# Performance work log

Measured on AMD Instinct MI355X. Metric: run time of the kernel, lower is better.

## Reference

```python
import jax
jax.config.update("jax_enable_x64", True)  # codes use *1e12 factors; need int64
import jax.numpy as jnp
import numpy as np

# HashRectsPt hyperparameters (module buffers)
W0, H0 = 512.0, 512.0
ALPHA = 1.2
GAMMA = 0.6
BX, BY = 0.5, 0.5
N_RECTS = 8192


def setup_inputs() -> dict:
    key = jax.random.key(0)
    k1, k2, k3 = jax.random.split(key, 3)
    xy = jax.random.uniform(k1, (N_RECTS, 2), minval=0.0, maxval=2000.0)
    wh = jax.random.uniform(k2, (N_RECTS, 2), minval=8.0, maxval=512.0)
    rects = jnp.concatenate([xy, wh], axis=1).astype(jnp.float32)  # [N,4] x,y,w,h
    conf = jax.random.uniform(k3, (N_RECTS,), dtype=jnp.float32)
    return {"rects": rects, "conf": conf}


def _hash_codes(rects):
    # HashRectsPt.__call__ -> packed single int64 code per rect
    x, y, w, h = rects[:, 0], rects[:, 1], rects[:, 2], rects[:, 3]
    log_alpha = jnp.log(jnp.float32(ALPHA))
    i = jnp.round((jnp.log(jnp.float32(W0)) - jnp.log(w)) / log_alpha)
    j = jnp.round((jnp.log(jnp.float32(H0)) - jnp.log(h)) / log_alpha)
    gamma_ratio = (1.0 - GAMMA) / (1.0 + GAMMA)
    di = (W0 * gamma_ratio) / (ALPHA ** i)
    dj = (H0 * gamma_ratio) / (ALPHA ** j)
    # b_is_relative=True branch
    qx = jnp.round(x / di - BX)
    qy = jnp.round(y / dj - BY)
    codes = (qx.astype(jnp.int64)
             + qy.astype(jnp.int64) * 10_000
             + i.astype(jnp.int64) * 100_000_000
             + j.astype(jnp.int64) * 1_000_000_000_000)
    return codes  # [N] int64


def reference(rects, conf):
    codes = _hash_codes(rects)                         # [N]
    n = codes.shape[0]
    # torch.unique with data-dependent U -> padded fixed-size unique (U<=N);
    # pad value can never equal a real code, so padded columns match nothing.
    uniq = jnp.unique(codes, size=n, fill_value=jnp.iinfo(jnp.int64).min)  # [N]
    assign = codes[:, None] == uniq[None, :]           # [N, U] bool
    scores = conf[:, None] * assign.astype(conf.dtype)  # [N, U]
    # torch .max(dim=0) returns first max index; jnp.argmax matches.
    argidx = jnp.argmax(scores, axis=0)                # [U]
    return argidx
```

## Files before the change

### kernel.cpp

```cpp
#include <hip/hip_runtime.h>
#include <math.h>

#define N     8192
#define TBL   16384
#define TBLM  16383

__device__ __forceinline__ unsigned int hash_code32(float x, float y, float w, float h) {
    const float LOG_ALPHA = (float)log((double)1.2f);
    const float LOGW0     = (float)log(512.0);
    float i_f = rintf((LOGW0 - (float)log((double)w)) / LOG_ALPHA);
    float j_f = rintf((LOGW0 - (float)log((double)h)) / LOG_ALPHA);
    float pi  = (float)pow((double)1.2f, (double)i_f);
    float pj  = (float)pow((double)1.2f, (double)j_f);
    float qx  = rintf(x / (128.0f / pi) - 0.5f);
    float qy  = rintf(y / (128.0f / pj) - 0.5f);
    return (unsigned int)qx
         | ((unsigned int)qy  << 11)
         | ((unsigned int)i_f << 22)
         | ((unsigned int)j_f << 27);
}

__device__ __forceinline__ unsigned int hslot(unsigned int code) {
    return (code * 2654435761u) >> 18;
}

__global__ void __launch_bounds__(256)
k_init(const float4* __restrict__ rects, const float* __restrict__ conf,
       unsigned long long* __restrict__ v64,
       unsigned int* __restrict__ tcode, unsigned long long* __restrict__ tkey,
       unsigned int* __restrict__ compact, unsigned int* __restrict__ cnt,
       int* __restrict__ out) {
    int gt = blockIdx.x * 256 + threadIdx.x;
    tcode[gt] = 0u;
    tkey[gt]  = 0ULL;
    if (gt < N) {
        float4 r = rects[gt];
        unsigned int code = hash_code32(r.x, r.y, r.z, r.w);
        v64[gt] = ((unsigned long long)code << 32)
                | (unsigned long long)__float_as_uint(conf[gt]);
        out[gt]     = 0;
        compact[gt] = 0xFFFFFFFFu;
    }
    if (gt == 0) *cnt = 0u;
}

__global__ void __launch_bounds__(64)
k_insert(const unsigned long long* __restrict__ v64,
         unsigned int* __restrict__ tcode,
         unsigned long long* __restrict__ tkey,
         unsigned int* __restrict__ compact,
         unsigned int* __restrict__ cnt) {
    int i = blockIdx.x * 64 + threadIdx.x;
    int lane = threadIdx.x;
    unsigned long long v = v64[i];
    unsigned int code = (unsigned int)(v >> 32);
    unsigned int tag  = code + 1u;
    unsigned int h = hslot(code);
    bool claimed = false;
    for (;;) {
        unsigned int prev = atomicCAS(&tcode[h], 0u, tag);
        if (prev == 0u) { claimed = true; break; }
        if (prev == tag) break;
        h = (h + 1) & TBLM;
    }
    atomicMax(&tkey[h], (v << 32) | (unsigned int)(N - 1 - i));
    unsigned long long mask = __ballot(claimed);
    if (mask) {
        int leader = __ffsll((long long)mask) - 1;
        unsigned int base = 0;
        if (lane == leader)
            base = atomicAdd(cnt, (unsigned int)__popcll(mask));
        base = (unsigned int)__shfl((int)base, leader);
        if (claimed) {
            unsigned int off = (unsigned int)__popcll(
                mask & ((1ULL << lane) - 1ULL));
            compact[base + off] = code;
        }
    }
}

__global__ void __launch_bounds__(512)
k_rank(const unsigned long long* __restrict__ v64,
       const unsigned int* __restrict__ tcode,
       const unsigned long long* __restrict__ tkey,
       const unsigned int* __restrict__ compact,
       int* __restrict__ out) {
    __shared__ unsigned int s_ci[32];
    __shared__ int s_part[8][32];
    const int t = threadIdx.x;
    const int b = blockIdx.x;
    if (t < 32) s_ci[t] = (unsigned int)(v64[b * 32 + t] >> 32);
    __syncthreads();

    const int g    = t >> 7;
    const int lt   = t & 127;
    const int wave = t >> 6;

    unsigned int ci[8];
    #pragma unroll
    for (int q = 0; q < 8; ++q)
        ci[q] = __builtin_amdgcn_readfirstlane(s_ci[g * 8 + q]);

    int r[8] = {0, 0, 0, 0, 0, 0, 0, 0};
    const uint4* c4 = (const uint4*)compact;
    #pragma unroll
    for (int k = 0; k < 16; ++k) {
        uint4 e = c4[lt + k * 128];
        #pragma unroll
        for (int q = 0; q < 8; ++q) {
            r[q] += (int)(e.x < ci[q]) + (int)(e.y < ci[q])
                  + (int)(e.z < ci[q]) + (int)(e.w < ci[q]);
        }
    }
    #pragma unroll
    for (int q = 0; q < 8; ++q) {
        r[q] += __shfl_xor(r[q], 1);
        r[q] += __shfl_xor(r[q], 2);
        r[q] += __shfl_xor(r[q], 4);
        r[q] += __shfl_xor(r[q], 8);
        r[q] += __shfl_xor(r[q], 16);
        r[q] += __shfl_xor(r[q], 32);
    }
    if ((t & 63) == 0) {
        #pragma unroll
        for (int q = 0; q < 8; ++q)
            s_part[wave][(wave >> 1) * 8 + q] = r[q];
    }
    __syncthreads();

    if (t < 32) {
        int i = b * 32 + t;
        int gg = t >> 3;
        int rr = s_part[2 * gg][t] + s_part[2 * gg + 1][t];
        unsigned long long vi = v64[i];
        unsigned int cI = (unsigned int)(vi >> 32);
        unsigned int h = hslot(cI);
        while (tcode[h] != cI + 1u) h = (h + 1) & TBLM;
        if ((unsigned int)tkey[h] == (unsigned int)(N - 1 - i)) {
            out[rr] = ((unsigned int)vi == 0u) ? 0 : i;
        }
    }
}

extern "C" void kernel_launch(void* const* d_in, const int* in_sizes, int n_in,
                              void* d_out, int out_size, void* d_ws, size_t ws_size,
                              hipStream_t stream) {
    const float4* rects = (const float4*)d_in[0];
    const float*  conf  = (const float*)d_in[1];
    int* out = (int*)d_out;

    char* ws = (char*)d_ws;
    unsigned long long* v64     = (unsigned long long*)ws;
    unsigned int*       tcode   = (unsigned int*)(ws + 65536);
    unsigned long long* tkey    = (unsigned long long*)(ws + 131072);
    unsigned int*       compact = (unsigned int*)(ws + 262144);
    unsigned int*       cnt     = (unsigned int*)(ws + 294912);

    k_init  <<<TBL / 256, 256, 0, stream>>>(rects, conf, v64, tcode, tkey,
                                            compact, cnt, out);
    k_insert<<<N / 64, 64, 0, stream>>>(v64, tcode, tkey, compact, cnt);
    k_rank  <<<256, 512, 0, stream>>>(v64, tcode, tkey, compact, out);
}
```

Measured before the change: 73.16 us.

## Drop init kernel using epoch-tagged persistent hash tables and per-slot compact

Removes the separate initialization kernel by keeping the hash table and key table in persistent device globals tagged with an epoch counter derived from a launch counter, so stale entries from earlier calls are treated as empty instead of being cleared. Code computation and insertion are fused into one kernel. A shuffle-based lookup table of powers of 1.2 replaces per-thread double pow. The compaction atomic is replaced by writing each code at its own index, with the unique count derived in the rank kernel, which also zero-fills the tail of the output. This saves a launch and the table clears, at the cost of CAS loops on 64-bit entries and reliance on epoch wraparound and the launch-counter arithmetic being correct.

```diff
diff --git a/kernel.cpp b/kernel.cpp
--- a/kernel.cpp
+++ b/kernel.cpp
@@ -1,92 +1,88 @@
 #include <hip/hip_runtime.h>
 #include <math.h>
 
-#define N     8192
-#define TBL   16384
-#define TBLM  16383
+#define N    8192
+#define TBL  16384
+#define TBLM 16383
+#define D1B  32
 
-__device__ __forceinline__ unsigned int hash_code32(float x, float y, float w, float h) {
-    const float LOG_ALPHA = (float)log((double)1.2f);
-    const float LOGW0     = (float)log(512.0);
-    float i_f = rintf((LOGW0 - (float)log((double)w)) / LOG_ALPHA);
-    float j_f = rintf((LOGW0 - (float)log((double)h)) / LOG_ALPHA);
-    float pi  = (float)pow((double)1.2f, (double)i_f);
-    float pj  = (float)pow((double)1.2f, (double)j_f);
-    float qx  = rintf(x / (128.0f / pi) - 0.5f);
-    float qy  = rintf(y / (128.0f / pj) - 0.5f);
-    return (unsigned int)qx
-         | ((unsigned int)qy  << 11)
-         | ((unsigned int)i_f << 22)
-         | ((unsigned int)j_f << 27);
-}
+__device__ unsigned long long g_tbl[TBL];
+__device__ unsigned long long g_tkey[TBL];
+__device__ unsigned int g_ctr;
+__device__ unsigned int g_cur;
 
 __device__ __forceinline__ unsigned int hslot(unsigned int code) {
     return (code * 2654435761u) >> 18;
 }
 
 __global__ void __launch_bounds__(256)
-k_init(const float4* __restrict__ rects, const float* __restrict__ conf,
-       unsigned long long* __restrict__ v64,
-       unsigned int* __restrict__ tcode, unsigned long long* __restrict__ tkey,
-       unsigned int* __restrict__ compact, unsigned int* __restrict__ cnt,
-       int* __restrict__ out) {
-    int gt = blockIdx.x * 256 + threadIdx.x;
-    tcode[gt] = 0u;
-    tkey[gt]  = 0ULL;
-    if (gt < N) {
-        float4 r = rects[gt];
-        unsigned int code = hash_code32(r.x, r.y, r.z, r.w);
-        v64[gt] = ((unsigned long long)code << 32)
-                | (unsigned long long)__float_as_uint(conf[gt]);
-        out[gt]     = 0;
-        compact[gt] = 0xFFFFFFFFu;
+k_insert(const float4* __restrict__ rects, const float* __restrict__ conf,
+         unsigned long long* __restrict__ v64,
+         unsigned int* __restrict__ compact) {
+    __shared__ unsigned int s_E;
+    const int t = threadIdx.x;
+    if (t == 0) {
+        unsigned int tk = atomicAdd(&g_ctr, 1u);
+        unsigned int E  = (tk >> 5) + 1u;
+        s_E  = E;
+        g_cur = E;
     }
-    if (gt == 0) *cnt = 0u;
-}
+    const int lane = t & 63;
+    float powL = (float)pow((double)1.2f, (double)(float)lane);
+    __syncthreads();
+    const unsigned int E = s_E;
 
-__global__ void __launch_bounds__(64)
-k_insert(const unsigned long long* __restrict__ v64,
-         unsigned int* __restrict__ tcode,
-         unsigned long long* __restrict__ tkey,
-         unsigned int* __restrict__ compact,
-         unsigned int* __restrict__ cnt) {
-    int i = blockIdx.x * 64 + threadIdx.x;
-    int lane = threadIdx.x;
-    unsigned long long v = v64[i];
-    unsigned int code = (unsigned int)(v >> 32);
-    unsigned int tag  = code + 1u;
+    const int i = blockIdx.x * 256 + t;
+    float4 r = rects[i];
+    const float LOG_ALPHA = (float)log((double)1.2f);
+    const float LOGW0     = (float)log(512.0);
+    float i_f = rintf((LOGW0 - (float)log((double)r.z)) / LOG_ALPHA);
+    float j_f = rintf((LOGW0 - (float)log((double)r.w)) / LOG_ALPHA);
+    float pi  = __shfl(powL, (int)i_f);
+    float pj  = __shfl(powL, (int)j_f);
+    float qx  = rintf(r.x / (128.0f / pi) - 0.5f);
+    float qy  = rintf(r.y / (128.0f / pj) - 0.5f);
+    unsigned int code = (unsigned int)qx | ((unsigned int)qy << 11)
+                      | ((unsigned int)i_f << 22) | ((unsigned int)j_f << 27);
+    unsigned int cb = __float_as_uint(conf[i]);
+    v64[i] = ((unsigned long long)code << 32) | cb;
+
+    unsigned long long want = ((unsigned long long)E << 32) | (code + 1u);
     unsigned int h = hslot(code);
     bool claimed = false;
     for (;;) {
-        unsigned int prev = atomicCAS(&tcode[h], 0u, tag);
-        if (prev == 0u) { claimed = true; break; }
-        if (prev == tag) break;
-        h = (h + 1) & TBLM;
+        unsigned long long cur = __hip_atomic_load(&g_tbl[h], __ATOMIC_RELAXED,
+                                                   __HIP_MEMORY_SCOPE_AGENT);
+        if (cur == want) break;
+        if ((unsigned int)(cur >> 32) == E) {
+            h = (h + 1) & TBLM;
+            continue;
+        }
+        unsigned long long prev = atomicCAS(&g_tbl[h], cur, want);
+        if (prev == cur)  { claimed = true; break; }
+        if (prev == want) break;
     }
-    atomicMax(&tkey[h], (v << 32) | (unsigned int)(N - 1 - i));
-    unsigned long long mask = __ballot(claimed);
-    if (mask) {
-        int leader = __ffsll((long long)mask) - 1;
-        unsigned int base = 0;
-        if (lane == leader)
-            base = atomicAdd(cnt, (unsigned int)__popcll(mask));
-        base = (unsigned int)__shfl((int)base, leader);
-        if (claimed) {
-            unsigned int off = (unsigned int)__popcll(
-                mask & ((1ULL << lane) - 1ULL));
-            compact[base + off] = code;
-        }
+    compact[i] = claimed ? code : 0xFFFFFFFFu;
+
+    unsigned long long etag = (unsigned long long)(E & 0x1FFFFFu) << 43;
+    unsigned long long mine = etag | ((unsigned long long)cb << 13)
+                            | (unsigned int)(8191 - i);
+    for (;;) {
+        unsigned long long cur = __hip_atomic_load(&g_tkey[h], __ATOMIC_RELAXED,
+                                                   __HIP_MEMORY_SCOPE_AGENT);
+        if ((cur >> 43) == (etag >> 43) && cur >= mine) break;
+        unsigned long long prev = atomicCAS(&g_tkey[h], cur, mine);
+        if (prev == cur) break;
     }
 }
 
 __global__ void __launch_bounds__(512)
 k_rank(const unsigned long long* __restrict__ v64,
-       const unsigned int* __restrict__ tcode,
-       const unsigned long long* __restrict__ tkey,
        const unsigned int* __restrict__ compact,
        int* __restrict__ out) {
     __shared__ unsigned int s_ci[32];
     __shared__ int s_part[8][32];
+    __shared__ int s_u[2];
     const int t = threadIdx.x;
     const int b = blockIdx.x;
     if (t < 32) s_ci[t] = (unsigned int)(v64[b * 32 + t] >> 32);
@@ -102,10 +98,13 @@
         ci[q] = __builtin_amdgcn_readfirstlane(s_ci[g * 8 + q]);
 
     int r[8] = {0, 0, 0, 0, 0, 0, 0, 0};
+    int u = 0;
     const uint4* c4 = (const uint4*)compact;
     #pragma unroll
     for (int k = 0; k < 16; ++k) {
         uint4 e = c4[lt + k * 128];
+        u += (int)(e.x != 0xFFFFFFFFu) + (int)(e.y != 0xFFFFFFFFu)
+           + (int)(e.z != 0xFFFFFFFFu) + (int)(e.w != 0xFFFFFFFFu);
         #pragma unroll
         for (int q = 0; q < 8; ++q) {
             r[q] += (int)(e.x < ci[q]) + (int)(e.y < ci[q])
@@ -121,24 +120,39 @@
         r[q] += __shfl_xor(r[q], 16);
         r[q] += __shfl_xor(r[q], 32);
     }
+    u += __shfl_xor(u, 1);  u += __shfl_xor(u, 2);  u += __shfl_xor(u, 4);
+    u += __shfl_xor(u, 8);  u += __shfl_xor(u, 16); u += __shfl_xor(u, 32);
     if ((t & 63) == 0) {
         #pragma unroll
         for (int q = 0; q < 8; ++q)
             s_part[wave][(wave >> 1) * 8 + q] = r[q];
+        if (wave < 2) s_u[wave] = u;
     }
     __syncthreads();
 
     if (t < 32) {
-        int i = b * 32 + t;
-        int gg = t >> 3;
-        int rr = s_part[2 * gg][t] + s_part[2 * gg + 1][t];
+        const int U  = s_u[0] + s_u[1];
+        const int i  = b * 32 + t;
+        const int gg = t >> 3;
+        const int rr = s_part[2 * gg][t] + s_part[2 * gg + 1][t];
+
         unsigned long long vi = v64[i];
         unsigned int cI = (unsigned int)(vi >> 32);
+        unsigned int E  = g_cur;
+        unsigned long long wantc = ((unsigned long long)E << 32) | (cI + 1u);
         unsigned int h = hslot(cI);
-        while (tcode[h] != cI + 1u) h = (h + 1) & TBLM;
-        if ((unsigned int)tkey[h] == (unsigned int)(N - 1 - i)) {
+        int steps = 0;
+        while (__hip_atomic_load(&g_tbl[h], __ATOMIC_RELAXED,
+                                 __HIP_MEMORY_SCOPE_AGENT) != wantc
+               && ++steps < TBL)
+            h = (h + 1) & TBLM;
+        unsigned long long wk = g_tkey[h];
+        bool iswin = ((wk >> 43) == (unsigned long long)(E & 0x1FFFFFu))
+                  && (((unsigned int)wk & 0x1FFFu) == (unsigned int)(8191 - i));
+        if (iswin)
             out[rr] = ((unsigned int)vi == 0u) ? 0 : i;
-        }
+        if (i >= U)
+            out[i] = 0;
     }
 }
 
@@ -151,13 +165,8 @@
 
     char* ws = (char*)d_ws;
     unsigned long long* v64     = (unsigned long long*)ws;
-    unsigned int*       tcode   = (unsigned int*)(ws + 65536);
-    unsigned long long* tkey    = (unsigned long long*)(ws + 131072);
-    unsigned int*       compact = (unsigned int*)(ws + 262144);
-    unsigned int*       cnt     = (unsigned int*)(ws + 294912);
+    unsigned int*       compact = (unsigned int*)(ws + 65536);
 
-    k_init  <<<TBL / 256, 256, 0, stream>>>(rects, conf, v64, tcode, tkey,
-                                            compact, cnt, out);
-    k_insert<<<N / 64, 64, 0, stream>>>(v64, tcode, tkey, compact, cnt);
-    k_rank  <<<256, 512, 0, stream>>>(v64, tcode, tkey, compact, out);
+    k_insert<<<D1B, 256, 0, stream>>>(rects, conf, v64, compact);
+    k_rank  <<<256, 512, 0, stream>>>(v64, compact, out);
 }
```

Measured after the change: 79.05 us. +8.0%, slower.

## Cache hash slots, tabulate alpha powers via shuffle, zero only unused outputs

Applied to the files above, without the earlier changes.

Replaces per-element double-precision pow with a per-lane table of 1.2^lane fetched by wave shuffle, which assumes i_f and j_f fall in 0..63. The insert kernel records each element's hash slot so the rank kernel no longer re-probes the table. Output zeroing moves from the init kernel to the rank kernel, which counts unique codes and zeroes only indices at or past that count. The main costs removed are the double pow in init and the probe loop in rank. In exchange, the rank kernel does an extra count pass over the compact array, and an extra slot buffer is written and read.

```diff
diff --git a/kernel.cpp b/kernel.cpp
--- a/kernel.cpp
+++ b/kernel.cpp
@@ -1,24 +1,9 @@
 #include <hip/hip_runtime.h>
 #include <math.h>
 
-#define N     8192
-#define TBL   16384
-#define TBLM  16383
-
-__device__ __forceinline__ unsigned int hash_code32(float x, float y, float w, float h) {
-    const float LOG_ALPHA = (float)log((double)1.2f);
-    const float LOGW0     = (float)log(512.0);
-    float i_f = rintf((LOGW0 - (float)log((double)w)) / LOG_ALPHA);
-    float j_f = rintf((LOGW0 - (float)log((double)h)) / LOG_ALPHA);
-    float pi  = (float)pow((double)1.2f, (double)i_f);
-    float pj  = (float)pow((double)1.2f, (double)j_f);
-    float qx  = rintf(x / (128.0f / pi) - 0.5f);
-    float qy  = rintf(y / (128.0f / pj) - 0.5f);
-    return (unsigned int)qx
-         | ((unsigned int)qy  << 11)
-         | ((unsigned int)i_f << 22)
-         | ((unsigned int)j_f << 27);
-}
+#define N    8192
+#define TBL  16384
+#define TBLM 16383
 
 __device__ __forceinline__ unsigned int hslot(unsigned int code) {
     return (code * 2654435761u) >> 18;
@@ -28,17 +13,27 @@
 k_init(const float4* __restrict__ rects, const float* __restrict__ conf,
        unsigned long long* __restrict__ v64,
        unsigned int* __restrict__ tcode, unsigned long long* __restrict__ tkey,
-       unsigned int* __restrict__ compact, unsigned int* __restrict__ cnt,
-       int* __restrict__ out) {
-    int gt = blockIdx.x * 256 + threadIdx.x;
+       unsigned int* __restrict__ compact, unsigned int* __restrict__ cnt) {
+    const int t  = threadIdx.x;
+    const int gt = blockIdx.x * 256 + t;
     tcode[gt] = 0u;
     tkey[gt]  = 0ULL;
     if (gt < N) {
+        const int lane = t & 63;
+        float powL = (float)pow((double)1.2f, (double)(float)lane);
         float4 r = rects[gt];
-        unsigned int code = hash_code32(r.x, r.y, r.z, r.w);
+        const float LOG_ALPHA = (float)log((double)1.2f);
+        const float LOGW0     = (float)log(512.0);
+        float i_f = rintf((LOGW0 - (float)log((double)r.z)) / LOG_ALPHA);
+        float j_f = rintf((LOGW0 - (float)log((double)r.w)) / LOG_ALPHA);
+        float pi  = __shfl(powL, (int)i_f);
+        float pj  = __shfl(powL, (int)j_f);
+        float qx  = rintf(r.x / (128.0f / pi) - 0.5f);
+        float qy  = rintf(r.y / (128.0f / pj) - 0.5f);
+        unsigned int code = (unsigned int)qx | ((unsigned int)qy << 11)
+                          | ((unsigned int)i_f << 22) | ((unsigned int)j_f << 27);
         v64[gt] = ((unsigned long long)code << 32)
                 | (unsigned long long)__float_as_uint(conf[gt]);
-        out[gt]     = 0;
         compact[gt] = 0xFFFFFFFFu;
     }
     if (gt == 0) *cnt = 0u;
@@ -49,7 +44,8 @@
          unsigned int* __restrict__ tcode,
          unsigned long long* __restrict__ tkey,
          unsigned int* __restrict__ compact,
-         unsigned int* __restrict__ cnt) {
+         unsigned int* __restrict__ cnt,
+         unsigned int* __restrict__ slot) {
     int i = blockIdx.x * 64 + threadIdx.x;
     int lane = threadIdx.x;
     unsigned long long v = v64[i];
@@ -63,6 +59,7 @@
         if (prev == tag) break;
         h = (h + 1) & TBLM;
     }
+    slot[i] = h;
     atomicMax(&tkey[h], (v << 32) | (unsigned int)(N - 1 - i));
     unsigned long long mask = __ballot(claimed);
     if (mask) {
@@ -81,12 +78,13 @@
 
 __global__ void __launch_bounds__(512)
 k_rank(const unsigned long long* __restrict__ v64,
-       const unsigned int* __restrict__ tcode,
        const unsigned long long* __restrict__ tkey,
        const unsigned int* __restrict__ compact,
+       const unsigned int* __restrict__ slot,
        int* __restrict__ out) {
     __shared__ unsigned int s_ci[32];
     __shared__ int s_part[8][32];
+    __shared__ int s_u[2];
     const int t = threadIdx.x;
     const int b = blockIdx.x;
     if (t < 32) s_ci[t] = (unsigned int)(v64[b * 32 + t] >> 32);
@@ -102,10 +100,13 @@
         ci[q] = __builtin_amdgcn_readfirstlane(s_ci[g * 8 + q]);
 
     int r[8] = {0, 0, 0, 0, 0, 0, 0, 0};
+    int u = 0;
     const uint4* c4 = (const uint4*)compact;
     #pragma unroll
     for (int k = 0; k < 16; ++k) {
         uint4 e = c4[lt + k * 128];
+        u += (int)(e.x != 0xFFFFFFFFu) + (int)(e.y != 0xFFFFFFFFu)
+           + (int)(e.z != 0xFFFFFFFFu) + (int)(e.w != 0xFFFFFFFFu);
         #pragma unroll
         for (int q = 0; q < 8; ++q) {
             r[q] += (int)(e.x < ci[q]) + (int)(e.y < ci[q])
@@ -121,24 +122,29 @@
         r[q] += __shfl_xor(r[q], 16);
         r[q] += __shfl_xor(r[q], 32);
     }
+    u += __shfl_xor(u, 1);  u += __shfl_xor(u, 2);  u += __shfl_xor(u, 4);
+    u += __shfl_xor(u, 8);  u += __shfl_xor(u, 16); u += __shfl_xor(u, 32);
     if ((t & 63) == 0) {
         #pragma unroll
         for (int q = 0; q < 8; ++q)
             s_part[wave][(wave >> 1) * 8 + q] = r[q];
+        if (wave < 2) s_u[wave] = u;
     }
     __syncthreads();
 
     if (t < 32) {
-        int i = b * 32 + t;
-        int gg = t >> 3;
-        int rr = s_part[2 * gg][t] + s_part[2 * gg + 1][t];
+        const int U  = s_u[0] + s_u[1];
+        const int i  = b * 32 + t;
+        const int gg = t >> 3;
+        const int rr = s_part[2 * gg][t] + s_part[2 * gg + 1][t];
+
         unsigned long long vi = v64[i];
-        unsigned int cI = (unsigned int)(vi >> 32);
-        unsigned int h = hslot(cI);
-        while (tcode[h] != cI + 1u) h = (h + 1) & TBLM;
-        if ((unsigned int)tkey[h] == (unsigned int)(N - 1 - i)) {
+        unsigned long long wk = tkey[slot[i]];
+        if ((unsigned int)wk == (unsigned int)(N - 1 - i)) {
             out[rr] = ((unsigned int)vi == 0u) ? 0 : i;
         }
+        if (i >= U)
+            out[i] = 0;
     }
 }
 
@@ -154,10 +160,11 @@
     unsigned int*       tcode   = (unsigned int*)(ws + 65536);
     unsigned long long* tkey    = (unsigned long long*)(ws + 131072);
     unsigned int*       compact = (unsigned int*)(ws + 262144);
-    unsigned int*       cnt     = (unsigned int*)(ws + 294912);
+    unsigned int*       slot    = (unsigned int*)(ws + 294912);
+    unsigned int*       cnt     = (unsigned int*)(ws + 327680);
 
     k_init  <<<TBL / 256, 256, 0, stream>>>(rects, conf, v64, tcode, tkey,
-                                            compact, cnt, out);
-    k_insert<<<N / 64, 64, 0, stream>>>(v64, tcode, tkey, compact, cnt);
-    k_rank  <<<256, 512, 0, stream>>>(v64, tcode, tkey, compact, out);
+                                            compact, cnt);
+    k_insert<<<N / 64, 64, 0, stream>>>(v64, tcode, tkey, compact, cnt, slot);
+    k_rank  <<<256, 512, 0, stream>>>(v64, tkey, compact, slot, out);
 }
```

Result: no change. 72.29 us (-1.2%).
